# Optimization experiments

Hardware: AMD Instinct MI355X
Metric: run time of the kernel (lower is better)

The kernel has to match this reference:

```python
import jax, jax.numpy as jnp
import numpy as np

JOINT_GROUPS = [[1, 2, 3], [4, 5, 6], [0, 7, 8, 9, 10], [11, 12, 13], [14, 15, 16]]
P_T = 9      # patch_size
C_OUT = 3    # out_channels
J = 17       # num_joints
HID = 512


def setup_inputs() -> dict:
    key = jax.random.key(0)
    ks = jax.random.split(key, 11)
    B, T_patches, G = 1024, 27, 5
    inp = {"tokens": jax.random.normal(ks[0], (B, T_patches, G, HID), dtype=jnp.float32)}
    for i, g in enumerate(JOINT_GROUPS):
        out_dim = P_T * len(g) * C_OUT
        inp[f"W{i}"] = jax.random.normal(ks[1 + 2 * i], (out_dim, HID), dtype=jnp.float32) * 0.02
        inp[f"b{i}"] = jax.random.normal(ks[2 + 2 * i], (out_dim,), dtype=jnp.float32) * 0.02
    return inp


def reference(tokens, W0, b0, W1, b1, W2, b2, W3, b3, W4, b4):
    Ws = [W0, W1, W2, W3, W4]
    bs = [b0, b1, b2, b3, b4]
    B, T_patches, G, H = tokens.shape
    T = T_patches * P_T  # 243
    output = jnp.zeros((B, T, J, C_OUT), dtype=tokens.dtype)
    count = jnp.zeros((B, T, J, 1), dtype=tokens.dtype)
    for i, group in enumerate(JOINT_GROUPS):
        gs = len(group)
        # (B, T_patches, H) @ (H, P_T*gs*C) -> (B, T_patches, P_T*gs*C)
        pred = jnp.einsum('bth,oh->bto', tokens[:, :, i, :], Ws[i]) + bs[i]
        pred = pred.reshape(B, T, gs, C_OUT)  # (B, T, gs, C)
        idx = jnp.array(group)
        output = output.at[:, :, idx, :].add(pred)
        count = count.at[:, :, idx, :].add(jnp.asarray(1.0, tokens.dtype))
    return output / jnp.clip(count, 1.0, None)
```

## Files before the change

### kernel.cpp

```cpp
#include <hip/hip_runtime.h>
#include <cstdint>


typedef __attribute__((ext_vector_type(8))) short short8;
typedef __attribute__((ext_vector_type(4))) float f32x4;
typedef __attribute__((ext_vector_type(4))) uint32_t u32x4;

constexpr int HID   = 512;
constexpr int TPCH  = 27;
constexpr int MROWS = 1024 * TPCH;
constexpr int RTOT  = 528;

struct Args {
  const float* W[5];
  const float* bias[5];
};

__device__ __forceinline__ uint32_t fbits(float x) {
  union { float f; uint32_t u; } v; v.f = x; return v.u;
}
__device__ __forceinline__ float bfloat(uint32_t u) {
  union { float f; uint32_t u; } v; v.u = u; return v.f;
}

__global__ __launch_bounds__(256) void convert_w(Args args, unsigned short* ws) {
  int idx = blockIdx.x * 256 + threadIdx.x;
  if (idx >= RTOT * HID) return;
  int nrow = idx >> 9;
  int k    = idx & (HID - 1);
  const float* Wg; int n; int nreal;
  if      (nrow < 96)  { Wg = args.W[0]; n = nrow;       nreal = 81;  }
  else if (nrow < 192) { Wg = args.W[1]; n = nrow - 96;  nreal = 81;  }
  else if (nrow < 336) { Wg = args.W[2]; n = nrow - 192; nreal = 135; }
  else if (nrow < 432) { Wg = args.W[3]; n = nrow - 336; nreal = 81;  }
  else                 { Wg = args.W[4]; n = nrow - 432; nreal = 81;  }
  float x = (n < nreal) ? Wg[(size_t)n * HID + k] : 0.f;
  uint32_t u = fbits(x);
  float r = x - bfloat(u & 0xFFFF0000u);
  ws[(size_t)nrow * 1024 + k]       = (unsigned short)(u >> 16);
  ws[(size_t)nrow * 1024 + 512 + k] = (unsigned short)(fbits(r) >> 16);
}

__device__ __forceinline__ short8 pack_hi(u32x4 a, u32x4 b) {
  union { uint32_t u[4]; short8 s; } cv;
  cv.u[0] = (a[0] >> 16) | (a[1] & 0xFFFF0000u);
  cv.u[1] = (a[2] >> 16) | (a[3] & 0xFFFF0000u);
  cv.u[2] = (b[0] >> 16) | (b[1] & 0xFFFF0000u);
  cv.u[3] = (b[2] >> 16) | (b[3] & 0xFFFF0000u);
  return cv.s;
}
__device__ __forceinline__ short8 pack_lo(u32x4 a, u32x4 b) {
  union { uint32_t u[4]; short8 s; } cv;
  #pragma unroll
  for (int p = 0; p < 4; ++p) {
    uint32_t u0 = (p < 2) ? a[2 * p]     : b[2 * (p - 2)];
    uint32_t u1 = (p < 2) ? a[2 * p + 1] : b[2 * (p - 2) + 1];
    float r0 = bfloat(u0) - bfloat(u0 & 0xFFFF0000u);
    float r1 = bfloat(u1) - bfloat(u1 & 0xFFFF0000u);
    cv.u[p] = (fbits(r0) >> 16) | (fbits(r1) & 0xFFFF0000u);
  }
  return cv.s;
}

template <int GS, int NR>
__device__ __forceinline__ void mfma_body(const float* __restrict__ tokens,
                                          const unsigned short* __restrict__ ws,
                                          const float* __restrict__ bias,
                                          float* __restrict__ out,
                                          int g, int rbase, int jbase) {
  constexpr int N = 27 * GS;
  const int lane = threadIdx.x & 63;
  const int wave = threadIdx.x >> 6;
  const int m0   = blockIdx.x * 128 + wave * 32;
  const int l15  = lane & 15;
  const int koff = (lane >> 4) * 8;

  f32x4 acc[2][NR];
  #pragma unroll
  for (int nr = 0; nr < NR; ++nr) {
    int n = nr * 16 + l15;
    float bv = (n < N) ? bias[n] : 0.f;
    f32x4 b4 = {bv, bv, bv, bv};
    acc[0][nr] = b4;
    acc[1][nr] = b4;
  }

  const float* aptr0 = tokens + (size_t)(m0 + l15) * (5 * HID) + g * HID + koff;
  const float* aptr1 = aptr0 + (size_t)16 * (5 * HID);
  const unsigned short* bbase = ws + (size_t)rbase * 1024 + koff;

  u32x4 c0a = *reinterpret_cast<const u32x4*>(aptr0);
  u32x4 c0b = *reinterpret_cast<const u32x4*>(aptr0 + 4);
  u32x4 c1a = *reinterpret_cast<const u32x4*>(aptr1);
  u32x4 c1b = *reinterpret_cast<const u32x4*>(aptr1 + 4);

  #pragma unroll 2
  for (int kc = 0; kc < 16; ++kc) {
    short8 bh[NR], bl[NR];
    #pragma unroll
    for (int nr = 0; nr < NR; ++nr) {
      const unsigned short* bp = bbase + (size_t)(nr * 16 + l15) * 1024 + kc * 32;
      bh[nr] = *reinterpret_cast<const short8*>(bp);
      bl[nr] = *reinterpret_cast<const short8*>(bp + 512);
    }
    const int kn = (kc + 1) & 15;
    u32x4 n0a = *reinterpret_cast<const u32x4*>(aptr0 + kn * 32);
    u32x4 n0b = *reinterpret_cast<const u32x4*>(aptr0 + kn * 32 + 4);
    u32x4 n1a = *reinterpret_cast<const u32x4*>(aptr1 + kn * 32);
    u32x4 n1b = *reinterpret_cast<const u32x4*>(aptr1 + kn * 32 + 4);
    short8 ah0 = pack_hi(c0a, c0b), al0 = pack_lo(c0a, c0b);
    short8 ah1 = pack_hi(c1a, c1b), al1 = pack_lo(c1a, c1b);
    #pragma unroll
    for (int nr = 0; nr < NR; ++nr) {
      acc[0][nr] = __builtin_amdgcn_mfma_f32_16x16x32_bf16(ah0, bh[nr], acc[0][nr], 0, 0, 0);
      acc[1][nr] = __builtin_amdgcn_mfma_f32_16x16x32_bf16(ah1, bh[nr], acc[1][nr], 0, 0, 0);
      acc[0][nr] = __builtin_amdgcn_mfma_f32_16x16x32_bf16(al0, bh[nr], acc[0][nr], 0, 0, 0);
      acc[1][nr] = __builtin_amdgcn_mfma_f32_16x16x32_bf16(al1, bh[nr], acc[1][nr], 0, 0, 0);
      acc[0][nr] = __builtin_amdgcn_mfma_f32_16x16x32_bf16(ah0, bl[nr], acc[0][nr], 0, 0, 0);
      acc[1][nr] = __builtin_amdgcn_mfma_f32_16x16x32_bf16(ah1, bl[nr], acc[1][nr], 0, 0, 0);
    }
    c0a = n0a; c0b = n0b; c1a = n1a; c1b = n1b;
  }

  #pragma unroll
  for (int mt = 0; mt < 2; ++mt) {
    int mrow = m0 + mt * 16 + (lane >> 4) * 4;
    #pragma unroll
    for (int nr = 0; nr < NR; ++nr) {
      int n = nr * 16 + l15;
      if (n < N) {
        int pt  = n / (3 * GS);
        int rem = n - pt * (3 * GS);
        int gl  = rem / 3;
        int c   = rem - gl * 3;
        int j   = (GS == 5) ? (gl == 0 ? 0 : gl + 6) : (jbase + gl);
        #pragma unroll
        for (int r = 0; r < 4; ++r) {
          int m  = mrow + r;
          int b  = m / TPCH;
          int tp = m - b * TPCH;
          out[((size_t)(b * 243 + tp * 9 + pt) * 17 + j) * 3 + c] = acc[mt][nr][r];
        }
      }
    }
  }
}

__global__ __launch_bounds__(256)
void decoder_mfma(const float* __restrict__ tokens, Args args,
                  const unsigned short* __restrict__ ws, float* __restrict__ out) {
  const int g = blockIdx.y;
  if (g == 2) {
    mfma_body<5, 9>(tokens, ws, args.bias[2], out, 2, 192, 0);
  } else {
    int jbase = (g == 0) ? 1 : (g == 1) ? 4 : (g == 3) ? 11 : 14;
    int rbase = (g == 0) ? 0 : (g == 1) ? 96 : (g == 3) ? 336 : 432;
    mfma_body<3, 6>(tokens, ws, args.bias[g], out, g, rbase, jbase);
  }
}

extern "C" void kernel_launch(void* const* d_in, const int* in_sizes, int n_in,
                              void* d_out, int out_size, void* d_ws, size_t ws_size,
                              hipStream_t stream) {
  const float* tokens = reinterpret_cast<const float*>(d_in[0]);
  Args args;
  for (int i = 0; i < 5; ++i) {
    args.W[i]    = reinterpret_cast<const float*>(d_in[1 + 2 * i]);
    args.bias[i] = reinterpret_cast<const float*>(d_in[2 + 2 * i]);
  }
  float* out = reinterpret_cast<float*>(d_out);
  unsigned short* ws = reinterpret_cast<unsigned short*>(d_ws);

  convert_w<<<(RTOT * HID + 255) / 256, 256, 0, stream>>>(args, ws);
  decoder_mfma<<<dim3(MROWS / 128, 5), 256, 0, stream>>>(tokens, args, ws, out);
}
```

Baseline: 527.2 us.

## Pre-swizzle split-bf16 weights into MFMA fragment order for coalesced loads

The weight conversion kernel now writes hi/lo bf16 fragments in the exact per-lane order the MFMA loop consumes, so each wave's B loads become contiguous 16-byte-per-lane reads instead of strided row reads. The GEMM kernel's indexing is updated to that layout, launch bounds request two blocks per CU, and the A prefetch no longer wraps to the first chunk on the last iteration. The layout change mainly improves load coalescing of the small, cache-resident weight matrix; the occupancy hint may constrain registers and cause spills given the large accumulator arrays.

```diff
diff --git a/kernel.cpp b/kernel.cpp
--- a/kernel.cpp
+++ b/kernel.cpp
@@ -9,7 +9,7 @@
 constexpr int HID   = 512;
 constexpr int TPCH  = 27;
 constexpr int MROWS = 1024 * TPCH;
-constexpr int RTOT  = 528;
+constexpr int FRAG_TOT = 67584;
 
 struct Args {
   const float* W[5];
@@ -21,24 +21,6 @@
 }
 __device__ __forceinline__ float bfloat(uint32_t u) {
   union { float f; uint32_t u; } v; v.u = u; return v.f;
-}
-
-__global__ __launch_bounds__(256) void convert_w(Args args, unsigned short* ws) {
-  int idx = blockIdx.x * 256 + threadIdx.x;
-  if (idx >= RTOT * HID) return;
-  int nrow = idx >> 9;
-  int k    = idx & (HID - 1);
-  const float* Wg; int n; int nreal;
-  if      (nrow < 96)  { Wg = args.W[0]; n = nrow;       nreal = 81;  }
-  else if (nrow < 192) { Wg = args.W[1]; n = nrow - 96;  nreal = 81;  }
-  else if (nrow < 336) { Wg = args.W[2]; n = nrow - 192; nreal = 135; }
-  else if (nrow < 432) { Wg = args.W[3]; n = nrow - 336; nreal = 81;  }
-  else                 { Wg = args.W[4]; n = nrow - 432; nreal = 81;  }
-  float x = (n < nreal) ? Wg[(size_t)n * HID + k] : 0.f;
-  uint32_t u = fbits(x);
-  float r = x - bfloat(u & 0xFFFF0000u);
-  ws[(size_t)nrow * 1024 + k]       = (unsigned short)(u >> 16);
-  ws[(size_t)nrow * 1024 + 512 + k] = (unsigned short)(fbits(r) >> 16);
 }
 
 __device__ __forceinline__ short8 pack_hi(u32x4 a, u32x4 b) {
@@ -62,12 +44,39 @@
   return cv.s;
 }
 
+__global__ __launch_bounds__(256) void convert_w(Args args, unsigned short* ws) {
+  int idx = blockIdx.x * 256 + threadIdx.x;
+  if (idx >= FRAG_TOT) return;
+  int f, NR, Nreal; const float* Wg;
+  if      (idx < 12288) { Wg = args.W[0]; f = idx;         NR = 6; Nreal = 81;  }
+  else if (idx < 24576) { Wg = args.W[1]; f = idx - 12288; NR = 6; Nreal = 81;  }
+  else if (idx < 43008) { Wg = args.W[2]; f = idx - 24576; NR = 9; Nreal = 135; }
+  else if (idx < 55296) { Wg = args.W[3]; f = idx - 43008; NR = 6; Nreal = 81;  }
+  else                  { Wg = args.W[4]; f = idx - 55296; NR = 6; Nreal = 81;  }
+  int lane = f & 63;
+  int rest = f >> 6;
+  int nr   = rest % NR;
+  int tmp  = rest / NR;
+  int h    = tmp & 1;
+  int kc   = tmp >> 1;
+  int n = nr * 16 + (lane & 15);
+  int k = kc * 32 + (lane >> 4) * 8;
+  u32x4 a = {0, 0, 0, 0}, b = {0, 0, 0, 0};
+  if (n < Nreal) {
+    const float* Wp = Wg + (size_t)n * HID + k;
+    a = *reinterpret_cast<const u32x4*>(Wp);
+    b = *reinterpret_cast<const u32x4*>(Wp + 4);
+  }
+  short8 frag = h ? pack_lo(a, b) : pack_hi(a, b);
+  *reinterpret_cast<short8*>(ws + (size_t)idx * 8) = frag;
+}
+
 template <int GS, int NR>
 __device__ __forceinline__ void mfma_body(const float* __restrict__ tokens,
                                           const unsigned short* __restrict__ ws,
                                           const float* __restrict__ bias,
                                           float* __restrict__ out,
-                                          int g, int rbase, int jbase) {
+                                          int g, int gfrag, int jbase) {
   constexpr int N = 27 * GS;
   const int lane = threadIdx.x & 63;
   const int wave = threadIdx.x >> 6;
@@ -87,7 +96,7 @@
 
   const float* aptr0 = tokens + (size_t)(m0 + l15) * (5 * HID) + g * HID + koff;
   const float* aptr1 = aptr0 + (size_t)16 * (5 * HID);
-  const unsigned short* bbase = ws + (size_t)rbase * 1024 + koff;
+  const unsigned short* bbase = ws + (size_t)gfrag + (size_t)lane * 8;
 
   u32x4 c0a = *reinterpret_cast<const u32x4*>(aptr0);
   u32x4 c0b = *reinterpret_cast<const u32x4*>(aptr0 + 4);
@@ -99,11 +108,11 @@
     short8 bh[NR], bl[NR];
     #pragma unroll
     for (int nr = 0; nr < NR; ++nr) {
-      const unsigned short* bp = bbase + (size_t)(nr * 16 + l15) * 1024 + kc * 32;
+      const unsigned short* bp = bbase + (size_t)((kc * 2) * NR + nr) * 512;
       bh[nr] = *reinterpret_cast<const short8*>(bp);
-      bl[nr] = *reinterpret_cast<const short8*>(bp + 512);
+      bl[nr] = *reinterpret_cast<const short8*>(bp + NR * 512);
     }
-    const int kn = (kc + 1) & 15;
+    const int kn = (kc + 1 < 16) ? kc + 1 : 15;
     u32x4 n0a = *reinterpret_cast<const u32x4*>(aptr0 + kn * 32);
     u32x4 n0b = *reinterpret_cast<const u32x4*>(aptr0 + kn * 32 + 4);
     u32x4 n1a = *reinterpret_cast<const u32x4*>(aptr1 + kn * 32);
@@ -146,16 +155,16 @@
   }
 }
 
-__global__ __launch_bounds__(256)
+__global__ __launch_bounds__(256, 2)
 void decoder_mfma(const float* __restrict__ tokens, Args args,
                   const unsigned short* __restrict__ ws, float* __restrict__ out) {
   const int g = blockIdx.y;
   if (g == 2) {
-    mfma_body<5, 9>(tokens, ws, args.bias[2], out, 2, 192, 0);
+    mfma_body<5, 9>(tokens, ws, args.bias[2], out, 2, 196608, 0);
   } else {
     int jbase = (g == 0) ? 1 : (g == 1) ? 4 : (g == 3) ? 11 : 14;
-    int rbase = (g == 0) ? 0 : (g == 1) ? 96 : (g == 3) ? 336 : 432;
-    mfma_body<3, 6>(tokens, ws, args.bias[g], out, g, rbase, jbase);
+    int gfrag = (g == 0) ? 0 : (g == 1) ? 98304 : (g == 3) ? 344064 : 442368;
+    mfma_body<3, 6>(tokens, ws, args.bias[g], out, g, gfrag, jbase);
   }
 }
 
@@ -171,6 +180,6 @@
   float* out = reinterpret_cast<float*>(d_out);
   unsigned short* ws = reinterpret_cast<unsigned short*>(d_ws);
 
-  convert_w<<<(RTOT * HID + 255) / 256, 256, 0, stream>>>(args, ws);
+  convert_w<<<(FRAG_TOT + 255) / 256, 256, 0, stream>>>(args, ws);
   decoder_mfma<<<dim3(MROWS / 128, 5), 256, 0, stream>>>(tokens, args, ws, out);
 }
```

Result: faster. 484.2 us (-8.2%).
